# Kernel optimization log

Hardware: AMD Instinct MI355X
Metric: run time of the kernel (lower is better)

Reference implementation:

```python
import jax, jax.numpy as jnp
import numpy as np

N = 50000          # nodes
E = 800000         # edges (before self loops)
G = 64             # graphs in batch
HEADS = 4
HID = 25
DENSE = HEADS * HID      # 100, must equal prototype feature dim
IN_DIM = 128
OUT_DIM = 2
NPC = 5                  # num_prototypes_per_class
NUM_PROT = OUT_DIM * NPC
EPS = 1e-4
NEG_SLOPE = 0.2


def setup_inputs() -> dict:
    key = jax.random.key(0)
    ks = jax.random.split(key, 20)
    x = jax.random.normal(ks[0], (N, IN_DIM), dtype=jnp.float32)
    edge_index = jax.random.randint(ks[1], (2, E), 0, N, dtype=jnp.int64)
    batch = jnp.sort(jax.random.randint(ks[2], (N,), 0, G, dtype=jnp.int64))
    inp = {"x": x, "edge_index": edge_index, "batch": batch}
    in_dims = [IN_DIM, DENSE, DENSE]
    for i in range(3):
        d = in_dims[i]
        s = 1.0 / np.sqrt(d)
        inp[f"W{i}"] = jax.random.uniform(ks[3 + 4 * i], (d, DENSE), jnp.float32, -s, s)
        inp[f"as{i}"] = jax.random.uniform(ks[4 + 4 * i], (HEADS, HID), jnp.float32, -s, s)
        inp[f"ad{i}"] = jax.random.uniform(ks[5 + 4 * i], (HEADS, HID), jnp.float32, -s, s)
        inp[f"b{i}"] = jnp.zeros((DENSE,), jnp.float32)
    inp["protos"] = jax.random.uniform(ks[16], (NUM_PROT, DENSE), jnp.float32)
    # last_layer weight: +1 for own class, -0.5 otherwise  [OUT_DIM, NUM_PROT]
    cls = jnp.arange(NUM_PROT) // NPC
    inp["last_w"] = jnp.where(cls[None, :] == jnp.arange(OUT_DIM)[:, None], 1.0, -0.5).astype(jnp.float32)
    return inp


def _gat_layer(x, src, dst, W, a_src, a_dst, b):
    h = (x @ W).reshape(N, HEADS, HID)                 # [N,H,D]
    e_src = jnp.einsum('nhd,hd->nh', h, a_src)         # [N,H]
    e_dst = jnp.einsum('nhd,hd->nh', h, a_dst)
    alpha = e_src[src] + e_dst[dst]                    # [Etot,H]
    alpha = jnp.where(alpha > 0, alpha, NEG_SLOPE * alpha)
    amax = jax.ops.segment_max(alpha, dst, num_segments=N)
    ex = jnp.exp(alpha - amax[dst])
    denom = jax.ops.segment_sum(ex, dst, num_segments=N)
    a = ex / (denom[dst] + 1e-16)                      # segmented softmax over in-edges
    msg = h[src] * a[:, :, None]                       # [Etot,H,D]
    out = jax.ops.segment_sum(msg, dst, num_segments=N)
    return out.reshape(N, DENSE) + b


def reference(x, edge_index, batch, W0, as0, ad0, b0, W1, as1, ad1, b1, W2, as2, ad2, b2, protos, last_w):
    loops = jnp.arange(N, dtype=edge_index.dtype)
    src = jnp.concatenate([edge_index[0], loops])      # PyG add_self_loops=True
    dst = jnp.concatenate([edge_index[1], loops])
    params = [(W0, as0, ad0, b0), (W1, as1, ad1, b1), (W2, as2, ad2, b2)]
    h = x
    for (W, a_s, a_d, b) in params:
        h = _gat_layer(h, src, dst, W, a_s, a_d, b)
        h = jax.nn.relu(h)
    node_emb = h
    graph_emb = jax.ops.segment_max(h, batch, num_segments=G)   # global_max_pool
    # prototype distances: squared euclidean via expansion
    xp = graph_emb @ protos.T                                    # [G,P]
    dist = -2.0 * xp + jnp.sum(graph_emb ** 2, axis=1, keepdims=True) + jnp.sum(protos ** 2, axis=1)[None, :]
    sim = jnp.log((dist + 1.0) / (dist + EPS))
    logits = sim @ last_w.T
    probs = jax.nn.softmax(logits, axis=-1)
    return logits, probs, node_emb, graph_emb, dist
```

## Files before the change

kernel.cpp:

```cpp
#include <hip/hip_runtime.h>
#include <hip/hip_bf16.h>

#define NN      50000
#define EE      800000
#define ETOT    (EE + NN)
#define GG      64
#define HEADS   4
#define HID     25
#define DENSE   100
#define IN_DIM  128
#define OUT_DIM 2
#define NPC     5
#define NUM_PROT (OUT_DIM * NPC)
#define NCHUNK  ((NN + 255) / 256)

#define NEG_INF (-3.402823466e38f)

__global__ void k_count(const int* __restrict__ ei, int* __restrict__ cnt, int* __restrict__ pos) {
    int e = blockIdx.x * blockDim.x + threadIdx.x;
    if (e >= ETOT) return;
    int dst = (e < EE) ? ei[EE + e] : (e - EE);
    pos[e] = atomicAdd(&cnt[dst], 1);
}

__global__ void k_scan1(const int* __restrict__ cnt, int* __restrict__ csum) {
    __shared__ int sh[256];
    int i = blockIdx.x * 256 + threadIdx.x;
    int v = (i < NN) ? cnt[i] : 0;
    sh[threadIdx.x] = v;
    __syncthreads();
    for (int s = 128; s > 0; s >>= 1) {
        if (threadIdx.x < s) sh[threadIdx.x] += sh[threadIdx.x + s];
        __syncthreads();
    }
    if (threadIdx.x == 0) csum[blockIdx.x] = sh[0];
}

__global__ void k_scan2(int* __restrict__ csum) {
    __shared__ int sh[256];
    int tid = threadIdx.x;
    int v = (tid < NCHUNK) ? csum[tid] : 0;
    sh[tid] = v;
    __syncthreads();
    for (int s = 1; s < 256; s <<= 1) {
        int t = (tid >= s) ? sh[tid - s] : 0;
        __syncthreads();
        sh[tid] += t;
        __syncthreads();
    }
    if (tid < NCHUNK) csum[tid] = sh[tid] - v;
    if (tid == NCHUNK) csum[NCHUNK] = sh[255];
}

__global__ void k_scan3(const int* __restrict__ cnt, const int* __restrict__ csum, int* __restrict__ offs) {
    __shared__ int sh[256];
    int i = blockIdx.x * 256 + threadIdx.x;
    int v = (i < NN) ? cnt[i] : 0;
    sh[threadIdx.x] = v;
    __syncthreads();
    for (int s = 1; s < 256; s <<= 1) {
        int t = (threadIdx.x >= s) ? sh[threadIdx.x - s] : 0;
        __syncthreads();
        sh[threadIdx.x] += t;
        __syncthreads();
    }
    int excl = sh[threadIdx.x] - v + csum[blockIdx.x];
    if (i <= NN) offs[i] = excl;
}

__global__ void k_scatter(const int* __restrict__ ei, const int* __restrict__ offs,
                          const int* __restrict__ pos, int* __restrict__ csr) {
    int e = blockIdx.x * blockDim.x + threadIdx.x;
    if (e >= ETOT) return;
    int src, dst;
    if (e < EE) { src = ei[e]; dst = ei[EE + e]; }
    else        { src = dst = e - EE; }
    csr[offs[dst] + pos[e]] = src;
}

__global__ void k_bounds(const int* __restrict__ batch, int* __restrict__ gstart) {
    int n = blockIdx.x * blockDim.x + threadIdx.x;
    if (n >= NN) return;
    int b = batch[n];
    if (n == 0) {
        for (int g = 0; g <= b; g++) gstart[g] = 0;
    } else {
        int pb = batch[n - 1];
        for (int g = pb + 1; g <= b; g++) gstart[g] = n;
    }
    if (n == NN - 1) {
        for (int g = b + 1; g <= GG; g++) gstart[g] = NN;
    }
}

template <int DIN>
__global__ __launch_bounds__(256) void k_gemm(const float* __restrict__ X,
                                              const float* __restrict__ W,
                                              float* __restrict__ H) {
    __shared__ float Ws[DIN * 102];
    const int tid = threadIdx.x;
    for (int idx = tid; idx < DIN * 100; idx += 256) {
        int k = idx / 100, c = idx - k * 100;
        Ws[k * 102 + c] = W[idx];
    }
    __syncthreads();

    const int wv = tid >> 6;
    const int lane = tid & 63;
    const int row0 = blockIdx.x * 64 + wv * 16;
    const int c0 = lane * 2;
    const bool act = (lane < 50);

    float accx[16], accy[16];
    #pragma unroll
    for (int r = 0; r < 16; ++r) { accx[r] = 0.f; accy[r] = 0.f; }

    for (int kq = 0; kq < DIN / 4; ++kq) {
        const int k0 = kq * 4;
        float2 wk0, wk1, wk2, wk3;
        if (act) {
            wk0 = *reinterpret_cast<const float2*>(&Ws[(k0 + 0) * 102 + c0]);
            wk1 = *reinterpret_cast<const float2*>(&Ws[(k0 + 1) * 102 + c0]);
            wk2 = *reinterpret_cast<const float2*>(&Ws[(k0 + 2) * 102 + c0]);
            wk3 = *reinterpret_cast<const float2*>(&Ws[(k0 + 3) * 102 + c0]);
        } else {
            wk0 = wk1 = wk2 = wk3 = float2{0.f, 0.f};
        }
        #pragma unroll
        for (int h = 0; h < 2; ++h) {
            float4 xv[8];
            #pragma unroll
            for (int r = 0; r < 8; ++r) {
                int row = row0 + h * 8 + r;
                int rc = (row < NN) ? row : (NN - 1);
                xv[r] = *reinterpret_cast<const float4*>(&X[(size_t)rc * DIN + k0]);
            }
            #pragma unroll
            for (int r = 0; r < 8; ++r) {
                int ar = h * 8 + r;
                accx[ar] += xv[r].x * wk0.x; accy[ar] += xv[r].x * wk0.y;
                accx[ar] += xv[r].y * wk1.x; accy[ar] += xv[r].y * wk1.y;
                accx[ar] += xv[r].z * wk2.x; accy[ar] += xv[r].z * wk2.y;
                accx[ar] += xv[r].w * wk3.x; accy[ar] += xv[r].w * wk3.y;
            }
        }
    }
    if (act) {
        #pragma unroll
        for (int r = 0; r < 16; ++r) {
            int row = row0 + r;
            if (row < NN) {
                float2 v = {accx[r], accy[r]};
                *reinterpret_cast<float2*>(&H[(size_t)row * 100 + c0]) = v;
            }
        }
    }
}

__global__ void k_esed(const float* __restrict__ H, const float* __restrict__ AS,
                       const float* __restrict__ AD, float* __restrict__ es, float* __restrict__ ed) {
    int t = blockIdx.x * blockDim.x + threadIdx.x;
    if (t >= NN * HEADS) return;
    int n = t >> 2, hd = t & 3;
    const float* hr = H + (size_t)n * 100 + hd * 25;
    const float* as = AS + hd * 25;
    const float* ad = AD + hd * 25;
    float s1 = 0.f, s2 = 0.f;
    #pragma unroll
    for (int d = 0; d < 25; d++) {
        float v = hr[d];
        s1 += v * as[d];
        s2 += v * ad[d];
    }
    es[t] = s1;
    ed[t] = s2;
}

__global__ __launch_bounds__(256) void k_msum(const float* __restrict__ es,
                                              const float* __restrict__ ed,
                                              const int* __restrict__ offs,
                                              const int* __restrict__ csr,
                                              float* __restrict__ wv) {
    int wid = threadIdx.x >> 6;
    int lane = threadIdx.x & 63;
    int n = blockIdx.x * 4 + wid;
    if (n >= NN) return;
    int el = lane >> 2, hd = lane & 3;
    int beg = offs[n], end = offs[n + 1];
    float edh = ed[n * 4 + hd];
    float m = NEG_INF, s = 0.f;
    for (int e = beg + el; e < end; e += 16) {
        int si = csr[e];
        float a = es[si * 4 + hd] + edh;
        a = (a > 0.f) ? a : 0.2f * a;
        float nm = fmaxf(m, a);
        float sc = __expf(m - nm);
        s = s * sc + __expf(a - nm);
        m = nm;
    }
    #pragma unroll
    for (int mask = 4; mask <= 32; mask <<= 1) {
        float mo = __shfl_xor(m, mask, 64);
        float so = __shfl_xor(s, mask, 64);
        float nm = fmaxf(m, mo);
        float f1 = (m  > NEG_INF) ? __expf(m  - nm) : 0.f;
        float f2 = (mo > NEG_INF) ? __expf(mo - nm) : 0.f;
        s = s * f1 + so * f2;
        m = nm;
    }
    float invs = 1.f / (s + 1e-16f);
    for (int e = beg + el; e < end; e += 16) {
        int si = csr[e];
        float a = es[si * 4 + hd] + edh;
        a = (a > 0.f) ? a : 0.2f * a;
        wv[(size_t)e * 4 + hd] = __expf(a - m) * invs;
    }
}

__global__ __launch_bounds__(128) void k_acc(const float* __restrict__ H,
                                             const float* __restrict__ wv,
                                             const int* __restrict__ offs,
                                             const int* __restrict__ csr,
                                             const float* __restrict__ bias,
                                             float* __restrict__ out) {
    int wid = threadIdx.x >> 6;
    int lane = threadIdx.x & 63;
    int n = blockIdx.x * 2 + wid;
    if (n >= NN || lane >= 50) return;
    int d0 = lane * 2;
    int h0 = d0 / 25, h1 = (d0 + 1) / 25;
    int beg = offs[n], end = offs[n + 1];
    float ax = 0.f, ay = 0.f;
    for (int e = beg; e < end; e += 8) {
        #pragma unroll
        for (int u = 0; u < 8; ++u) {
            int ee = e + u;
            int ec = (ee < end) ? ee : beg;
            int idx = csr[ec];
            float wx = wv[ec * 4 + h0];
            float wy = wv[ec * 4 + h1];
            if (ee >= end) { wx = 0.f; wy = 0.f; }
            float2 xv = *reinterpret_cast<const float2*>(&H[idx * 100 + d0]);
            ax += wx * xv.x;
            ay += wy * xv.y;
        }
    }
    float2 b = *reinterpret_cast<const float2*>(&bias[d0]);
    float2 o = {fmaxf(ax + b.x, 0.f), fmaxf(ay + b.y, 0.f)};
    *reinterpret_cast<float2*>(&out[n * 100 + d0]) = o;
}

__global__ void k_pool1(const float* __restrict__ NE, const int* __restrict__ gstart,
                        float* __restrict__ part) {
    int g = blockIdx.x >> 3, c = blockIdx.x & 7;
    int d = threadIdx.x;
    if (d >= 100) return;
    int s0 = gstart[g], s1 = gstart[g + 1];
    int len = s1 - s0;
    int n0 = s0 + (int)((long long)len * c / 8);
    int n1 = s0 + (int)((long long)len * (c + 1) / 8);
    float vm = NEG_INF;
    for (int n = n0; n < n1; n++) vm = fmaxf(vm, NE[(size_t)n * 100 + d]);
    part[(size_t)(g * 8 + c) * 100 + d] = vm;
}

__global__ void k_pool2(const float* __restrict__ part, float* __restrict__ GE) {
    int g = blockIdx.x;
    int d = threadIdx.x;
    if (d >= 100) return;
    float vm = NEG_INF;
    for (int c = 0; c < 8; c++) vm = fmaxf(vm, part[(size_t)(g * 8 + c) * 100 + d]);
    GE[(size_t)g * 100 + d] = vm;
}

__global__ void k_head(const float* __restrict__ GE, const float* __restrict__ P,
                       const float* __restrict__ LW, float* __restrict__ logits,
                       float* __restrict__ probs, float* __restrict__ dist) {
    int g = blockIdx.x;
    __shared__ float ge[100];
    __shared__ float sims[NUM_PROT];
    __shared__ float lg[OUT_DIM];
    int t = threadIdx.x;
    if (t < 100) ge[t] = GE[(size_t)g * 100 + t];
    __syncthreads();
    if (t < NUM_PROT) {
        float dot = 0.f, pn = 0.f, gn = 0.f;
        for (int d = 0; d < 100; d++) {
            float pv = P[t * 100 + d];
            float gv = ge[d];
            dot += gv * pv;
            pn += pv * pv;
            gn += gv * gv;
        }
        float ds = gn - 2.f * dot + pn;
        dist[g * NUM_PROT + t] = ds;
        sims[t] = logf((ds + 1.f) / (ds + 1e-4f));
    }
    __syncthreads();
    if (t < OUT_DIM) {
        float l = 0.f;
        for (int p = 0; p < NUM_PROT; p++) l += sims[p] * LW[t * NUM_PROT + p];
        lg[t] = l;
        logits[g * OUT_DIM + t] = l;
    }
    __syncthreads();
    if (t == 0) {
        float mm = fmaxf(lg[0], lg[1]);
        float e0 = __expf(lg[0] - mm), e1 = __expf(lg[1] - mm);
        float inv = 1.f / (e0 + e1);
        probs[g * OUT_DIM + 0] = e0 * inv;
        probs[g * OUT_DIM + 1] = e1 * inv;
    }
}

extern "C" void kernel_launch(void* const* d_in, const int* in_sizes, int n_in,
                              void* d_out, int out_size, void* d_ws, size_t ws_size,
                              hipStream_t stream) {
    const float* x     = (const float*)d_in[0];
    const int*   ei    = (const int*)d_in[1];
    const int*   batch = (const int*)d_in[2];
    const float* Wm[3]  = {(const float*)d_in[3],  (const float*)d_in[7],  (const float*)d_in[11]};
    const float* ASm[3] = {(const float*)d_in[4],  (const float*)d_in[8],  (const float*)d_in[12]};
    const float* ADm[3] = {(const float*)d_in[5],  (const float*)d_in[9],  (const float*)d_in[13]};
    const float* Bm[3]  = {(const float*)d_in[6],  (const float*)d_in[10], (const float*)d_in[14]};
    const float* P  = (const float*)d_in[15];
    const float* LW = (const float*)d_in[16];

    float* out = (float*)d_out;
    float* logits  = out;
    float* probs   = out + GG * OUT_DIM;
    float* nodeEmb = out + 2 * GG * OUT_DIM;
    float* GE      = nodeEmb + (size_t)NN * DENSE;
    float* disto   = GE + GG * DENSE;

    char* w = (char*)d_ws;
    size_t off = 0;
    auto carve = [&](size_t bytes) -> void* {
        void* p = w + off;
        off += (bytes + 15) & ~(size_t)15;
        return p;
    };
    float* hA   = (float*)carve((size_t)NN * DENSE * 4);
    float* es   = (float*)carve((size_t)NN * HEADS * 4);
    float* ed   = (float*)carve((size_t)NN * HEADS * 4);
    int* cnt    = (int*)carve((size_t)NN * 4);
    int* offs   = (int*)carve((size_t)(NN + 1) * 4);
    int* pos    = (int*)carve((size_t)ETOT * 4);
    int* csr    = (int*)carve((size_t)ETOT * 4);
    int* csum   = (int*)carve((size_t)(NCHUNK + 1) * 4);
    int* gstart = (int*)carve((size_t)(GG + 1) * 4);
    float* part = (float*)carve((size_t)GG * 8 * DENSE * 4);
    float* wv   = (float*)carve((size_t)ETOT * HEADS * 4);
    (void)in_sizes; (void)n_in; (void)out_size; (void)ws_size;

    hipMemsetAsync(cnt, 0, (size_t)NN * 4, stream);
    k_count<<<(ETOT + 255) / 256, 256, 0, stream>>>(ei, cnt, pos);
    k_scan1<<<NCHUNK, 256, 0, stream>>>(cnt, csum);
    k_scan2<<<1, 256, 0, stream>>>(csum);
    k_scan3<<<NCHUNK, 256, 0, stream>>>(cnt, csum, offs);
    k_scatter<<<(ETOT + 255) / 256, 256, 0, stream>>>(ei, offs, pos, csr);
    k_bounds<<<(NN + 255) / 256, 256, 0, stream>>>(batch, gstart);

    const int gemmGrid = (NN + 63) / 64;
    const int esedGrid = (NN * HEADS + 255) / 256;
    const int msumGrid = (NN + 3) / 4;
    const int accGrid  = (NN + 1) / 2;

    const float* layerIn = x;
    for (int l = 0; l < 3; ++l) {
        if (l == 0) k_gemm<IN_DIM><<<gemmGrid, 256, 0, stream>>>(layerIn, Wm[l], hA);
        else        k_gemm<DENSE ><<<gemmGrid, 256, 0, stream>>>(layerIn, Wm[l], hA);
        k_esed<<<esedGrid, 256, 0, stream>>>(hA, ASm[l], ADm[l], es, ed);
        k_msum<<<msumGrid, 256, 0, stream>>>(es, ed, offs, csr, wv);
        k_acc<<<accGrid, 128, 0, stream>>>(hA, wv, offs, csr, Bm[l], nodeEmb);
        layerIn = nodeEmb;
    }

    k_pool1<<<GG * 8, 128, 0, stream>>>(nodeEmb, gstart, part);
    k_pool2<<<GG, 128, 0, stream>>>(part, GE);

    k_head<<<GG, 128, 0, stream>>>(GE, P, LW, logits, probs, disto);
}
```

Before: 532.7 us.

## Replace tiled shared-memory GEMM with one-row-per-wave GEMV reading weights from cache

Replaces the shared-memory-staged GEMM (64 rows per block, 16 rows per wave, register accumulators) with a kernel in which each wave computes a single output row. X is read as broadcast float4 loads and W is read straight from global memory through the cache. This removes the per-block weight staging, the barrier and the heavy register pressure, and raises the block count. The cost is that W is no longer reused from registers across rows, so every row re-reads the whole weight matrix from L1/L2.

```diff
diff --git a/kernel.cpp b/kernel.cpp
--- a/kernel.cpp
+++ b/kernel.cpp
@@ -94,66 +94,32 @@
 }
 
 template <int DIN>
-__global__ __launch_bounds__(256) void k_gemm(const float* __restrict__ X,
-                                              const float* __restrict__ W,
-                                              float* __restrict__ H) {
-    __shared__ float Ws[DIN * 102];
-    const int tid = threadIdx.x;
-    for (int idx = tid; idx < DIN * 100; idx += 256) {
-        int k = idx / 100, c = idx - k * 100;
-        Ws[k * 102 + c] = W[idx];
-    }
-    __syncthreads();
-
-    const int wv = tid >> 6;
-    const int lane = tid & 63;
-    const int row0 = blockIdx.x * 64 + wv * 16;
-    const int c0 = lane * 2;
-    const bool act = (lane < 50);
-
-    float accx[16], accy[16];
-    #pragma unroll
-    for (int r = 0; r < 16; ++r) { accx[r] = 0.f; accy[r] = 0.f; }
-
-    for (int kq = 0; kq < DIN / 4; ++kq) {
-        const int k0 = kq * 4;
-        float2 wk0, wk1, wk2, wk3;
-        if (act) {
-            wk0 = *reinterpret_cast<const float2*>(&Ws[(k0 + 0) * 102 + c0]);
-            wk1 = *reinterpret_cast<const float2*>(&Ws[(k0 + 1) * 102 + c0]);
-            wk2 = *reinterpret_cast<const float2*>(&Ws[(k0 + 2) * 102 + c0]);
-            wk3 = *reinterpret_cast<const float2*>(&Ws[(k0 + 3) * 102 + c0]);
-        } else {
-            wk0 = wk1 = wk2 = wk3 = float2{0.f, 0.f};
-        }
-        #pragma unroll
-        for (int h = 0; h < 2; ++h) {
-            float4 xv[8];
-            #pragma unroll
-            for (int r = 0; r < 8; ++r) {
-                int row = row0 + h * 8 + r;
-                int rc = (row < NN) ? row : (NN - 1);
-                xv[r] = *reinterpret_cast<const float4*>(&X[(size_t)rc * DIN + k0]);
-            }
-            #pragma unroll
-            for (int r = 0; r < 8; ++r) {
-                int ar = h * 8 + r;
-                accx[ar] += xv[r].x * wk0.x; accy[ar] += xv[r].x * wk0.y;
-                accx[ar] += xv[r].y * wk1.x; accy[ar] += xv[r].y * wk1.y;
-                accx[ar] += xv[r].z * wk2.x; accy[ar] += xv[r].z * wk2.y;
-                accx[ar] += xv[r].w * wk3.x; accy[ar] += xv[r].w * wk3.y;
-            }
-        }
-    }
-    if (act) {
-        #pragma unroll
-        for (int r = 0; r < 16; ++r) {
-            int row = row0 + r;
-            if (row < NN) {
-                float2 v = {accx[r], accy[r]};
-                *reinterpret_cast<float2*>(&H[(size_t)row * 100 + c0]) = v;
-            }
-        }
+__global__ __launch_bounds__(256) void k_gemmv(const float* __restrict__ X,
+                                               const float* __restrict__ W,
+                                               float* __restrict__ H) {
+    const int wid  = __builtin_amdgcn_readfirstlane(threadIdx.x >> 6);
+    const int lane = threadIdx.x & 63;
+    const int row  = blockIdx.x * 4 + wid;
+    const int c0   = lane * 2;
+    const int cl   = (lane < 50) ? c0 : 98;
+    const float* xr = X + (size_t)row * DIN;
+    float a0x = 0.f, a0y = 0.f, a1x = 0.f, a1y = 0.f;
+    float a2x = 0.f, a2y = 0.f, a3x = 0.f, a3y = 0.f;
+    #pragma unroll 4
+    for (int k = 0; k < DIN; k += 4) {
+        float4 xv = *reinterpret_cast<const float4*>(xr + k);
+        float2 w0 = *reinterpret_cast<const float2*>(&W[(size_t)(k + 0) * 100 + cl]);
+        float2 w1 = *reinterpret_cast<const float2*>(&W[(size_t)(k + 1) * 100 + cl]);
+        float2 w2 = *reinterpret_cast<const float2*>(&W[(size_t)(k + 2) * 100 + cl]);
+        float2 w3 = *reinterpret_cast<const float2*>(&W[(size_t)(k + 3) * 100 + cl]);
+        a0x += xv.x * w0.x; a0y += xv.x * w0.y;
+        a1x += xv.y * w1.x; a1y += xv.y * w1.y;
+        a2x += xv.z * w2.x; a2y += xv.z * w2.y;
+        a3x += xv.w * w3.x; a3y += xv.w * w3.y;
+    }
+    if (lane < 50) {
+        float2 o = {a0x + a1x + a2x + a3x, a0y + a1y + a2y + a3y};
+        *reinterpret_cast<float2*>(&H[(size_t)row * 100 + c0]) = o;
     }
 }
 
@@ -361,15 +327,15 @@
     k_scatter<<<(ETOT + 255) / 256, 256, 0, stream>>>(ei, offs, pos, csr);
     k_bounds<<<(NN + 255) / 256, 256, 0, stream>>>(batch, gstart);
 
-    const int gemmGrid = (NN + 63) / 64;
+    const int gemmGrid = NN / 4;
     const int esedGrid = (NN * HEADS + 255) / 256;
     const int msumGrid = (NN + 3) / 4;
     const int accGrid  = (NN + 1) / 2;
 
     const float* layerIn = x;
     for (int l = 0; l < 3; ++l) {
-        if (l == 0) k_gemm<IN_DIM><<<gemmGrid, 256, 0, stream>>>(layerIn, Wm[l], hA);
-        else        k_gemm<DENSE ><<<gemmGrid, 256, 0, stream>>>(layerIn, Wm[l], hA);
+        if (l == 0) k_gemmv<IN_DIM><<<gemmGrid, 256, 0, stream>>>(layerIn, Wm[l], hA);
+        else        k_gemmv<DENSE ><<<gemmGrid, 256, 0, stream>>>(layerIn, Wm[l], hA);
         k_esed<<<esedGrid, 256, 0, stream>>>(hA, ASm[l], ADm[l], es, ed);
         k_msum<<<msumGrid, 256, 0, stream>>>(es, ed, offs, csr, wv);
         k_acc<<<accGrid, 128, 0, stream>>>(hA, wv, offs, csr, Bm[l], nodeEmb);
```

New measurement: 796.5 us. 49.5% more time.

## Restructure node GEMM to keep weight column in registers with prefetched rows

Applied to the files above, without the earlier changes.

The projection GEMM no longer stages W in shared memory. Each of 128 threads now holds one full weight column in registers (one output column per thread) and loops over 8 row groups of 8 rows, double-buffering the X row loads. The aim is to remove LDS traffic and the block-wide sync. In exchange, X rows are loaded as the same address across every lane of a wave (broadcast loads), register pressure rises a lot (up to 128 weight floats per thread), and 28 of 128 threads sit idle.

```diff
diff --git a/kernel.cpp b/kernel.cpp
--- a/kernel.cpp
+++ b/kernel.cpp
@@ -94,67 +94,67 @@
 }
 
 template <int DIN>
-__global__ __launch_bounds__(256) void k_gemm(const float* __restrict__ X,
-                                              const float* __restrict__ W,
-                                              float* __restrict__ H) {
-    __shared__ float Ws[DIN * 102];
+__device__ __forceinline__ void gemmw_body(const float* __restrict__ X,
+                                           const float* __restrict__ W,
+                                           float* __restrict__ H) {
+    constexpr int KQ = DIN / 4;
     const int tid = threadIdx.x;
-    for (int idx = tid; idx < DIN * 100; idx += 256) {
-        int k = idx / 100, c = idx - k * 100;
-        Ws[k * 102 + c] = W[idx];
-    }
-    __syncthreads();
-
-    const int wv = tid >> 6;
-    const int lane = tid & 63;
-    const int row0 = blockIdx.x * 64 + wv * 16;
-    const int c0 = lane * 2;
-    const bool act = (lane < 50);
-
-    float accx[16], accy[16];
+    const bool act = (tid < 100);
+    const int cc = act ? tid : 99;
+    const int row0 = blockIdx.x * 64;
+
+    float wreg[DIN];
     #pragma unroll
-    for (int r = 0; r < 16; ++r) { accx[r] = 0.f; accy[r] = 0.f; }
-
-    for (int kq = 0; kq < DIN / 4; ++kq) {
-        const int k0 = kq * 4;
-        float2 wk0, wk1, wk2, wk3;
-        if (act) {
-            wk0 = *reinterpret_cast<const float2*>(&Ws[(k0 + 0) * 102 + c0]);
-            wk1 = *reinterpret_cast<const float2*>(&Ws[(k0 + 1) * 102 + c0]);
-            wk2 = *reinterpret_cast<const float2*>(&Ws[(k0 + 2) * 102 + c0]);
-            wk3 = *reinterpret_cast<const float2*>(&Ws[(k0 + 3) * 102 + c0]);
-        } else {
-            wk0 = wk1 = wk2 = wk3 = float2{0.f, 0.f};
-        }
+    for (int k = 0; k < DIN; ++k) wreg[k] = W[(size_t)k * 100 + cc];
+
+    for (int rg = 0; rg < 8; ++rg) {
+        const int r0 = row0 + rg * 8;
+        const float* xp[8];
         #pragma unroll
-        for (int h = 0; h < 2; ++h) {
-            float4 xv[8];
-            #pragma unroll
-            for (int r = 0; r < 8; ++r) {
-                int row = row0 + h * 8 + r;
-                int rc = (row < NN) ? row : (NN - 1);
-                xv[r] = *reinterpret_cast<const float4*>(&X[(size_t)rc * DIN + k0]);
+        for (int r = 0; r < 8; ++r) {
+            int rr = r0 + r; if (rr >= NN) rr = NN - 1;
+            xp[r] = X + (size_t)rr * DIN;
+        }
+        float acc[8] = {};
+        float4 buf[2][8];
+        #pragma unroll
+        for (int r = 0; r < 8; ++r)
+            buf[0][r] = *reinterpret_cast<const float4*>(xp[r]);
+        #pragma unroll
+        for (int kq = 0; kq < KQ; ++kq) {
+            const int cur = kq & 1, nxt = cur ^ 1;
+            if (kq + 1 < KQ) {
+                #pragma unroll
+                for (int r = 0; r < 8; ++r)
+                    buf[nxt][r] = *reinterpret_cast<const float4*>(xp[r] + (kq + 1) * 4);
             }
             #pragma unroll
             for (int r = 0; r < 8; ++r) {
-                int ar = h * 8 + r;
-                accx[ar] += xv[r].x * wk0.x; accy[ar] += xv[r].x * wk0.y;
-                accx[ar] += xv[r].y * wk1.x; accy[ar] += xv[r].y * wk1.y;
-                accx[ar] += xv[r].z * wk2.x; accy[ar] += xv[r].z * wk2.y;
-                accx[ar] += xv[r].w * wk3.x; accy[ar] += xv[r].w * wk3.y;
+                float4 xv = buf[cur][r];
+                acc[r] += xv.x * wreg[kq * 4 + 0];
+                acc[r] += xv.y * wreg[kq * 4 + 1];
+                acc[r] += xv.z * wreg[kq * 4 + 2];
+                acc[r] += xv.w * wreg[kq * 4 + 3];
             }
         }
-    }
-    if (act) {
-        #pragma unroll
-        for (int r = 0; r < 16; ++r) {
-            int row = row0 + r;
-            if (row < NN) {
-                float2 v = {accx[r], accy[r]};
-                *reinterpret_cast<float2*>(&H[(size_t)row * 100 + c0]) = v;
+        if (act) {
+            #pragma unroll
+            for (int r = 0; r < 8; ++r) {
+                int rr = r0 + r;
+                if (rr < NN) H[(size_t)rr * 100 + tid] = acc[r];
             }
         }
     }
+}
+
+__global__ __launch_bounds__(128) void k_gemm0(const float* __restrict__ X, const float* __restrict__ W, float* __restrict__ H) {
+    gemmw_body<IN_DIM>(X, W, H);
+}
+__global__ __launch_bounds__(128) void k_gemm1(const float* __restrict__ X, const float* __restrict__ W, float* __restrict__ H) {
+    gemmw_body<DENSE>(X, W, H);
+}
+__global__ __launch_bounds__(128) void k_gemm2(const float* __restrict__ X, const float* __restrict__ W, float* __restrict__ H) {
+    gemmw_body<DENSE>(X, W, H);
 }
 
 __global__ void k_esed(const float* __restrict__ H, const float* __restrict__ AS,
@@ -368,8 +368,9 @@
 
     const float* layerIn = x;
     for (int l = 0; l < 3; ++l) {
-        if (l == 0) k_gemm<IN_DIM><<<gemmGrid, 256, 0, stream>>>(layerIn, Wm[l], hA);
-        else        k_gemm<DENSE ><<<gemmGrid, 256, 0, stream>>>(layerIn, Wm[l], hA);
+        if (l == 0)      k_gemm0<<<gemmGrid, 128, 0, stream>>>(layerIn, Wm[l], hA);
+        else if (l == 1) k_gemm1<<<gemmGrid, 128, 0, stream>>>(layerIn, Wm[l], hA);
+        else             k_gemm2<<<gemmGrid, 128, 0, stream>>>(layerIn, Wm[l], hA);
         k_esed<<<esedGrid, 256, 0, stream>>>(hA, ASm[l], ADm[l], es, ed);
         k_msum<<<msumGrid, 256, 0, stream>>>(es, ed, offs, csr, wv);
         k_acc<<<accGrid, 128, 0, stream>>>(hA, wv, offs, csr, Bm[l], nodeEmb);
```

New measurement: 556.9 us. 4.6% more time.
